# Performance work log

Hardware: AMD Instinct MI355X
Metric: run time of the kernel (lower is better)

Reference implementation:

```python
import jax, jax.numpy as jnp
import numpy as np

B, N, D = 8, 128, 768  # batch, max_units, input_dim
F = 3 * D + 2 * N - 1  # cat(2D) + multi(D) + rel_pos(2N-1)


def setup_inputs() -> dict:
    key = jax.random.key(0)
    k1, k2, k3, k4 = jax.random.split(key, 4)
    input_tensor = jax.random.normal(k1, (B, N, D), dtype=jnp.float32)
    unit_mask = jax.random.randint(k2, (B, N), 0, 2).astype(jnp.int32)
    # Linear(F, 1): weight [F], bias [1], init uniform(-0.05, 0.05) as in torch code
    W = jax.random.uniform(k3, (F,), minval=-0.05, maxval=0.05, dtype=jnp.float32)
    b = jax.random.uniform(k4, (1,), minval=-0.05, maxval=0.05, dtype=jnp.float32)
    return {"input_tensor": input_tensor, "W": W, "b": b, "unit_mask": unit_mask}


def reference(input_tensor, W, b, unit_mask):
    # Pair row (i, j) = [h_i ; h_j ; h_i*h_j ; onehot(j - i + N - 1)]
    # score[b,i,j] = h_i.w1 + h_j.w2 + (h_i*wm).h_j + wr[j-i+N-1] + bias
    # This is mathematically identical to building the [B,N,N,F] pair matrix
    # and applying Linear(F,1), but fused / never materialized.
    d = input_tensor.shape[-1]
    n = input_tensor.shape[1]
    w1, w2, wm, wr = W[:d], W[d:2 * d], W[2 * d:3 * d], W[3 * d:]

    si = input_tensor @ w1                                   # [B, N]  (h_i block)
    sj = input_tensor @ w2                                   # [B, N]  (h_j block)
    sm = jnp.einsum('bid,bjd->bij', input_tensor * wm, input_tensor)  # multi block
    idx = jnp.arange(n)
    rel = wr[idx[None, :] - idx[:, None] + n - 1]            # [N, N] rel-pos block

    scores = si[:, :, None] + sj[:, None, :] + sm + rel[None, :, :] + b[0]

    m = unit_mask.astype(bool)
    pair_mask = m[:, :, None] & m[:, None, :]                # row i valid AND col j valid
    neg_inf = jnp.array(-jnp.inf, dtype=scores.dtype)
    return jnp.where(pair_mask, scores, neg_inf)
```

## Files before the change

kernel.cpp:

```cpp
#include <hip/hip_runtime.h>


#define D 768
#define N 128
#define NEG_BIG (-3.0e38f)

typedef __attribute__((ext_vector_type(8))) short bf16x8;
typedef __attribute__((ext_vector_type(4))) float f32x4;
typedef __attribute__((ext_vector_type(4))) short short4v;

static __device__ __forceinline__ unsigned short f2bf(float f) {
  unsigned int u = __float_as_uint(f);
  return (unsigned short)((u + 0x7fffu + ((u >> 16) & 1u)) >> 16);
}

__global__ __launch_bounds__(256) void prep_k(const float* __restrict__ X,
                                              const float* __restrict__ W,
                                              float* __restrict__ ws) {
  const int lane = threadIdx.x & 63;
  const int wid  = threadIdx.x >> 6;
  const int row  = blockIdx.x * 4 + wid;
  const float* xr = X + row * D;
  const float* w1 = W;
  const float* w2 = W + D;
  const float* wm = W + 2 * D;
  unsigned short* Xb = (unsigned short*)(ws + 2048);
  unsigned short* Am = Xb + 8 * N * D;

  float s1 = 0.f, s2 = 0.f;
#pragma unroll
  for (int t = 0; t < 3; ++t) {
    const int k = (t * 64 + lane) * 4;
    const float4 xv = *reinterpret_cast<const float4*>(xr + k);
    const float4 av = *reinterpret_cast<const float4*>(w1 + k);
    const float4 bv = *reinterpret_cast<const float4*>(w2 + k);
    const float4 mv = *reinterpret_cast<const float4*>(wm + k);
    s1 += xv.x * av.x + xv.y * av.y + xv.z * av.z + xv.w * av.w;
    s2 += xv.x * bv.x + xv.y * bv.y + xv.z * bv.z + xv.w * bv.w;
    short4v xs, ms;
    xs.x = (short)f2bf(xv.x); xs.y = (short)f2bf(xv.y);
    xs.z = (short)f2bf(xv.z); xs.w = (short)f2bf(xv.w);
    ms.x = (short)f2bf(xv.x * mv.x); ms.y = (short)f2bf(xv.y * mv.y);
    ms.z = (short)f2bf(xv.z * mv.z); ms.w = (short)f2bf(xv.w * mv.w);
    *reinterpret_cast<short4v*>(Xb + row * D + k) = xs;
    *reinterpret_cast<short4v*>(Am + row * D + k) = ms;
  }
#pragma unroll
  for (int off = 32; off > 0; off >>= 1) {
    s1 += __shfl_down(s1, off, 64);
    s2 += __shfl_down(s2, off, 64);
  }
  if (lane == 0) {
    ws[row]        = s1;
    ws[1024 + row] = s2;
  }
}

__global__ __launch_bounds__(64) void mm_k(const float* __restrict__ W,
                                           const float* __restrict__ bptr,
                                           const int* __restrict__ mask,
                                           const float* __restrict__ ws,
                                           float* __restrict__ out) {
  const int lane = threadIdx.x;
  const int nt   = blockIdx.x;
  const int mt   = blockIdx.y;
  const int b    = blockIdx.z;
  const int r    = lane & 15;
  const int g    = lane >> 4;

  const unsigned short* Xb = (const unsigned short*)(ws + 2048);
  const unsigned short* Am = Xb + 8 * N * D;
  const unsigned short* arow = Am + (b * N + mt * 16 + r) * D + g * 8;
  const unsigned short* brow = Xb + (b * N + nt * 16 + r) * D + g * 8;

  f32x4 acc = {0.f, 0.f, 0.f, 0.f};
#pragma unroll
  for (int kk = 0; kk < D / 32; ++kk) {
    const bf16x8 av = *reinterpret_cast<const bf16x8*>(arow + kk * 32);
    const bf16x8 bv = *reinterpret_cast<const bf16x8*>(brow + kk * 32);
    acc = __builtin_amdgcn_mfma_f32_16x16x32_bf16(av, bv, acc, 0, 0, 0);
  }

  const float b0  = bptr[0];
  const int   j   = nt * 16 + r;
  const int   mj  = mask[b * N + j];
  const float sjv = ws[1024 + b * N + j];
  const float* wr = W + 3 * D;
#pragma unroll
  for (int q = 0; q < 4; ++q) {
    const int   i  = mt * 16 + g * 4 + q;
    const int   mi = mask[b * N + i];
    const float v  = acc[q] + ws[b * N + i] + sjv + wr[j - i + N - 1] + b0;
    out[(b * N + i) * N + j] = (mi && mj) ? v : NEG_BIG;
  }
}

extern "C" void kernel_launch(void* const* d_in, const int* in_sizes, int n_in,
                              void* d_out, int out_size, void* d_ws, size_t ws_size,
                              hipStream_t stream) {
  const float* X    = (const float*)d_in[0];
  const float* W    = (const float*)d_in[1];
  const float* bptr = (const float*)d_in[2];
  const int*   mask = (const int*)d_in[3];
  float* out = (float*)d_out;
  float* ws  = (float*)d_ws;

  prep_k<<<256, 256, 0, stream>>>(X, W, ws);
  mm_k<<<dim3(8, 8, 8), 64, 0, stream>>>(W, bptr, mask, ws, out);
}
```

Measured before the change: 14.68 us.

## Fuse bf16 prep and MFMA score kernels into a single launch

Merges the preprocessing kernel (row dot products with w1/w2 and bf16 conversion of X and X*wm) into the MFMA tile kernel, so each block reads fp32 X directly and converts on the fly. This removes one kernel launch and the round trip of the bf16 copies through workspace memory. In exchange, every tile recomputes conversions and row dot products redundantly (each row is reprocessed by 8 tiles) and reads fp32 rather than bf16, doubling per-tile load bytes, which mostly hit in cache.

New measurement: 15.39 us. +4.9%, slower.

```diff
diff --git a/kernel.cpp b/kernel.cpp
--- a/kernel.cpp
+++ b/kernel.cpp
@@ -1,4 +1,5 @@
 #include <hip/hip_runtime.h>
+#include <hip/hip_bf16.h>
 
 
 #define D 768
@@ -7,90 +8,87 @@
 
 typedef __attribute__((ext_vector_type(8))) short bf16x8;
 typedef __attribute__((ext_vector_type(4))) float f32x4;
-typedef __attribute__((ext_vector_type(4))) short short4v;
 
-static __device__ __forceinline__ unsigned short f2bf(float f) {
-  unsigned int u = __float_as_uint(f);
-  return (unsigned short)((u + 0x7fffu + ((u >> 16) & 1u)) >> 16);
+static __device__ __forceinline__ short b16(float f) {
+  union { __hip_bfloat16 h; short s; } u;
+  u.h = __float2bfloat16(f);
+  return u.s;
 }
 
-__global__ __launch_bounds__(256) void prep_k(const float* __restrict__ X,
+__global__ __launch_bounds__(64) void fused_k(const float* __restrict__ X,
                                               const float* __restrict__ W,
-                                              float* __restrict__ ws) {
-  const int lane = threadIdx.x & 63;
-  const int wid  = threadIdx.x >> 6;
-  const int row  = blockIdx.x * 4 + wid;
-  const float* xr = X + row * D;
-  const float* w1 = W;
-  const float* w2 = W + D;
-  const float* wm = W + 2 * D;
-  unsigned short* Xb = (unsigned short*)(ws + 2048);
-  unsigned short* Am = Xb + 8 * N * D;
+                                              const float* __restrict__ bptr,
+                                              const int* __restrict__ mask,
+                                              float* __restrict__ out) {
+  __shared__ float sils[16];
+  const int lane = threadIdx.x;
+  const int nt = blockIdx.x;
+  const int mt = blockIdx.y;
+  const int b  = blockIdx.z;
+  const int r  = lane & 15;
+  const int g  = lane >> 4;
 
-  float s1 = 0.f, s2 = 0.f;
-#pragma unroll
-  for (int t = 0; t < 3; ++t) {
-    const int k = (t * 64 + lane) * 4;
-    const float4 xv = *reinterpret_cast<const float4*>(xr + k);
-    const float4 av = *reinterpret_cast<const float4*>(w1 + k);
-    const float4 bv = *reinterpret_cast<const float4*>(w2 + k);
-    const float4 mv = *reinterpret_cast<const float4*>(wm + k);
-    s1 += xv.x * av.x + xv.y * av.y + xv.z * av.z + xv.w * av.w;
-    s2 += xv.x * bv.x + xv.y * bv.y + xv.z * bv.z + xv.w * bv.w;
-    short4v xs, ms;
-    xs.x = (short)f2bf(xv.x); xs.y = (short)f2bf(xv.y);
-    xs.z = (short)f2bf(xv.z); xs.w = (short)f2bf(xv.w);
-    ms.x = (short)f2bf(xv.x * mv.x); ms.y = (short)f2bf(xv.y * mv.y);
-    ms.z = (short)f2bf(xv.z * mv.z); ms.w = (short)f2bf(xv.w * mv.w);
-    *reinterpret_cast<short4v*>(Xb + row * D + k) = xs;
-    *reinterpret_cast<short4v*>(Am + row * D + k) = ms;
-  }
-#pragma unroll
-  for (int off = 32; off > 0; off >>= 1) {
-    s1 += __shfl_down(s1, off, 64);
-    s2 += __shfl_down(s2, off, 64);
-  }
-  if (lane == 0) {
-    ws[row]        = s1;
-    ws[1024 + row] = s2;
-  }
-}
-
-__global__ __launch_bounds__(64) void mm_k(const float* __restrict__ W,
-                                           const float* __restrict__ bptr,
-                                           const int* __restrict__ mask,
-                                           const float* __restrict__ ws,
-                                           float* __restrict__ out) {
-  const int lane = threadIdx.x;
-  const int nt   = blockIdx.x;
-  const int mt   = blockIdx.y;
-  const int b    = blockIdx.z;
-  const int r    = lane & 15;
-  const int g    = lane >> 4;
-
-  const unsigned short* Xb = (const unsigned short*)(ws + 2048);
-  const unsigned short* Am = Xb + 8 * N * D;
-  const unsigned short* arow = Am + (b * N + mt * 16 + r) * D + g * 8;
-  const unsigned short* brow = Xb + (b * N + nt * 16 + r) * D + g * 8;
+  const float* xa = X + (b * N + mt * 16 + r) * D + g * 8;
+  const float* xb = X + (b * N + nt * 16 + r) * D + g * 8;
+  const float* w1 = W + g * 8;
+  const float* w2 = W + D + g * 8;
+  const float* wm = W + 2 * D + g * 8;
 
   f32x4 acc = {0.f, 0.f, 0.f, 0.f};
-#pragma unroll
-  for (int kk = 0; kk < D / 32; ++kk) {
-    const bf16x8 av = *reinterpret_cast<const bf16x8*>(arow + kk * 32);
-    const bf16x8 bv = *reinterpret_cast<const bf16x8*>(brow + kk * 32);
-    acc = __builtin_amdgcn_mfma_f32_16x16x32_bf16(av, bv, acc, 0, 0, 0);
+  float sa = 0.f, sb = 0.f;
+
+#pragma unroll 4
+  for (int kk = 0; kk < D; kk += 32) {
+    const float4 a0 = *reinterpret_cast<const float4*>(xa + kk);
+    const float4 a1 = *reinterpret_cast<const float4*>(xa + kk + 4);
+    const float4 b0v = *reinterpret_cast<const float4*>(xb + kk);
+    const float4 b1v = *reinterpret_cast<const float4*>(xb + kk + 4);
+    const float4 m0 = *reinterpret_cast<const float4*>(wm + kk);
+    const float4 m1 = *reinterpret_cast<const float4*>(wm + kk + 4);
+    const float4 u0 = *reinterpret_cast<const float4*>(w1 + kk);
+    const float4 u1 = *reinterpret_cast<const float4*>(w1 + kk + 4);
+    const float4 v0 = *reinterpret_cast<const float4*>(w2 + kk);
+    const float4 v1 = *reinterpret_cast<const float4*>(w2 + kk + 4);
+
+    sa = fmaf(a0.x, u0.x, sa); sa = fmaf(a0.y, u0.y, sa);
+    sa = fmaf(a0.z, u0.z, sa); sa = fmaf(a0.w, u0.w, sa);
+    sa = fmaf(a1.x, u1.x, sa); sa = fmaf(a1.y, u1.y, sa);
+    sa = fmaf(a1.z, u1.z, sa); sa = fmaf(a1.w, u1.w, sa);
+    sb = fmaf(b0v.x, v0.x, sb); sb = fmaf(b0v.y, v0.y, sb);
+    sb = fmaf(b0v.z, v0.z, sb); sb = fmaf(b0v.w, v0.w, sb);
+    sb = fmaf(b1v.x, v1.x, sb); sb = fmaf(b1v.y, v1.y, sb);
+    sb = fmaf(b1v.z, v1.z, sb); sb = fmaf(b1v.w, v1.w, sb);
+
+    bf16x8 af, bf;
+    af[0] = b16(a0.x * m0.x); af[1] = b16(a0.y * m0.y);
+    af[2] = b16(a0.z * m0.z); af[3] = b16(a0.w * m0.w);
+    af[4] = b16(a1.x * m1.x); af[5] = b16(a1.y * m1.y);
+    af[6] = b16(a1.z * m1.z); af[7] = b16(a1.w * m1.w);
+    bf[0] = b16(b0v.x); bf[1] = b16(b0v.y);
+    bf[2] = b16(b0v.z); bf[3] = b16(b0v.w);
+    bf[4] = b16(b1v.x); bf[5] = b16(b1v.y);
+    bf[6] = b16(b1v.z); bf[7] = b16(b1v.w);
+
+    acc = __builtin_amdgcn_mfma_f32_16x16x32_bf16(af, bf, acc, 0, 0, 0);
   }
 
-  const float b0  = bptr[0];
+  sa += __shfl_xor(sa, 16, 64);
+  sa += __shfl_xor(sa, 32, 64);
+  sb += __shfl_xor(sb, 16, 64);
+  sb += __shfl_xor(sb, 32, 64);
+  if (g == 0) sils[r] = sa;
+  __syncthreads();
+  const float4 siq = *reinterpret_cast<const float4*>(&sils[g * 4]);
+
+  const float b0s = bptr[0];
   const int   j   = nt * 16 + r;
   const int   mj  = mask[b * N + j];
-  const float sjv = ws[1024 + b * N + j];
   const float* wr = W + 3 * D;
 #pragma unroll
   for (int q = 0; q < 4; ++q) {
     const int   i  = mt * 16 + g * 4 + q;
     const int   mi = mask[b * N + i];
-    const float v  = acc[q] + ws[b * N + i] + sjv + wr[j - i + N - 1] + b0;
+    const float v  = acc[q] + (&siq.x)[q] + sb + wr[j - i + N - 1] + b0s;
     out[(b * N + i) * N + j] = (mi && mj) ? v : NEG_BIG;
   }
 }
@@ -103,8 +101,6 @@
   const float* bptr = (const float*)d_in[2];
   const int*   mask = (const int*)d_in[3];
   float* out = (float*)d_out;
-  float* ws  = (float*)d_ws;
 
-  prep_k<<<256, 256, 0, stream>>>(X, W, ws);
-  mm_k<<<dim3(8, 8, 8), 64, 0, stream>>>(W, bptr, mask, ws, out);
+  fused_k<<<dim3(8, 8, 8), 64, 0, stream>>>(X, W, bptr, mask, out);
 }
```
